# Optimization experiments

Hardware: AMD Instinct MI355X
Metric: run time of the kernel (lower is better)

Reference implementation:

```python
import jax, jax.numpy as jnp
import numpy as np

NEG_INF = -1e30


def setup_inputs() -> dict:
    key = jax.random.key(0)
    ks = jax.random.split(key, 7)
    B, D, LC, LQ = 32, 128, 2048, 256
    C = jax.random.normal(ks[0], (B, D, LC), dtype=jnp.float32)
    Q = jax.random.normal(ks[1], (B, D, LQ), dtype=jnp.float32)
    Cmask = jax.random.randint(ks[2], (B, LC), 0, 2, dtype=jnp.int32)
    Qmask = jax.random.randint(ks[3], (B, LQ), 0, 2, dtype=jnp.int32)
    w4C = jax.random.normal(ks[4], (D, 1), dtype=jnp.float32) * (6.0 / (D + 1)) ** 0.5
    w4Q = jax.random.normal(ks[5], (D, 1), dtype=jnp.float32) * (6.0 / (D + 1)) ** 0.5
    w4mlu = jax.random.normal(ks[6], (1, 1, D), dtype=jnp.float32) * (6.0 / (D + 1)) ** 0.5
    bias = jnp.zeros((1,), dtype=jnp.float32)
    return {"C": C, "Q": Q, "Cmask": Cmask, "Qmask": Qmask,
            "w4C": w4C, "w4Q": w4Q, "w4mlu": w4mlu, "bias": bias}


def reference(C, Q, Cmask, Qmask, w4C, w4Q, w4mlu, bias):
    # C: [B, D, Lc], Q: [B, D, Lq] -> transpose to token-major
    Ct = jnp.swapaxes(C, 1, 2)  # [B, Lc, D]
    Qt = jnp.swapaxes(Q, 1, 2)  # [B, Lq, D]
    # trilinear similarity S[b,i,j] = w4C.Ct[b,i] + w4Q.Qt[b,j] + (Ct[b,i]*w4mlu).Qt[b,j] + bias
    sub0 = Ct @ w4C                                   # [B, Lc, 1]
    sub1 = jnp.swapaxes(Qt @ w4Q, 1, 2)               # [B, 1, Lq]
    sub2 = jnp.einsum('bcd,bqd->bcq', Ct * w4mlu, Qt)  # [B, Lc, Lq]
    S = sub0 + sub1 + sub2 + bias                     # [B, Lc, Lq]
    Qm = Qmask.astype(jnp.float32)[:, None, :]        # [B, 1, Lq]
    Cm = Cmask.astype(jnp.float32)[:, :, None]        # [B, Lc, 1]
    S1 = jax.nn.softmax(S + NEG_INF * (1.0 - Qm), axis=2)  # row softmax over Lq
    S2 = jax.nn.softmax(S + NEG_INF * (1.0 - Cm), axis=1)  # col softmax over Lc
    A = S1 @ Qt                                       # [B, Lc, D]
    Bt = jnp.einsum('bcq,bkq->bck', S1, S2) @ Ct      # (S1 @ S2^T) @ C -> [B, Lc, D]
    out = jnp.concatenate([Ct, A, Ct * A, Ct * Bt], axis=2)  # [B, Lc, 4D]
    return jnp.swapaxes(out, 1, 2)  # [B, 4D, Lc]
```

## Files before the change

kernel.cpp:

```cpp
#include <hip/hip_runtime.h>
#include <cstdint>


#define NB 32
#define ND 128
#define NLC 2048
#define NLQ 256
#define FNEG (-1.0e30f)
#define ESHIFT 20.0f

typedef __attribute__((ext_vector_type(8))) short bf16x8;
typedef __attribute__((ext_vector_type(4))) float f32x4;
#define MFMA16(a, b, c) __builtin_amdgcn_mfma_f32_16x16x32_bf16(a, b, c, 0, 0, 0)

__device__ __forceinline__ short f2bf(float x) {
  union { float f; unsigned u; } v; v.f = x;
  unsigned r = (v.u + 0x7FFFu + ((v.u >> 16) & 1u)) >> 16;
  return (short)r;
}
__device__ __forceinline__ float bf2f(short x) {
  union { unsigned u; float f; } v; v.u = ((unsigned)(unsigned short)x) << 16;
  return v.f;
}

__global__ __launch_bounds__(256) void k_tr(const float* __restrict__ C,
                                            const float* __restrict__ Q,
                                            const float* __restrict__ w4C,
                                            const float* __restrict__ w4Q,
                                            const float* __restrict__ w4mlu,
                                            short* __restrict__ Cfr,
                                            short* __restrict__ Cafr,
                                            short* __restrict__ Qfr,
                                            short* __restrict__ Qbf,
                                            float* __restrict__ cqp,
                                            float* __restrict__ qqp,
                                            const int* __restrict__ Qmask,
                                            short* __restrict__ mskE) {
  __shared__ float T[32][66];
  const int b = blockIdx.z, d0 = blockIdx.y * 32;
  const int t = threadIdx.x;
  const bool isC = blockIdx.x < 32;
  const int i0 = (isC ? blockIdx.x : (blockIdx.x - 32)) * 64;
  const int L = isC ? NLC : NLQ;
  const float* in = isC ? C : Q;
#pragma unroll
  for (int rr = 0; rr < 2; ++rr) {
    int idx = t + rr * 256;
    int dd = idx >> 4, c4 = idx & 15;
    const float* src = in + ((size_t)b * ND + d0 + dd) * L + i0 + c4 * 4;
    float4 v = *(const float4*)src;
    T[dd][c4 * 4 + 0] = v.x;
    T[dd][c4 * 4 + 1] = v.y;
    T[dd][c4 * 4 + 2] = v.z;
    T[dd][c4 * 4 + 3] = v.w;
    if (!isC) {
      short4 o;
      o.x = f2bf(v.x); o.y = f2bf(v.y); o.z = f2bf(v.z); o.w = f2bf(v.w);
      *(short4*)(Qbf + ((size_t)b * ND + d0 + dd) * L + i0 + c4 * 4) = o;
    }
  }
  __syncthreads();
  if (t < 64) {
    const float* wd_ = isC ? w4C : w4Q;
    float s = 0.f;
#pragma unroll
    for (int dd = 0; dd < 32; ++dd) s = fmaf(T[dd][t], wd_[d0 + dd], s);
    (isC ? cqp : qqp)[((size_t)blockIdx.y * NB + b) * L + i0 + t] = s;
  }
  if (!isC && blockIdx.y == 0 && t < 64) {
    const int j = i0 + t;
    mskE[(size_t)b * NLQ + j] = Qmask[b * NLQ + j] ? (short)0xFFFF : (short)0;
  }
  if (isC) {
    const int dt_loc = t & 1, ic_loc = (t >> 1) & 1, lane = t >> 2;
    const int dd = dt_loc * 16 + (lane & 15);
    const int ibase = ic_loc * 32 + ((lane >> 4) & 3) * 8;
    bf16x8 pk;
#pragma unroll
    for (int k = 0; k < 8; ++k) pk[k] = f2bf(T[dd][ibase + k]);
    const size_t dtile = (size_t)((d0 >> 4) + dt_loc);
    const size_t ichunk = (size_t)((i0 >> 5) + ic_loc);
    *(bf16x8*)(Cafr + (((size_t)b * 8 + dtile) * (size_t)(NLC >> 5) + ichunk) * 512 +
               (size_t)lane * 8) = pk;
  }
  const int i = t >> 2, seg = t & 3;
  bf16x8 pack;
#pragma unroll
  for (int k = 0; k < 8; ++k) {
    int d = seg * 8 + k;
    float x = T[d][i];
    if (!isC) x *= w4mlu[d0 + d];
    pack[k] = f2bf(x);
  }
  {
    const size_t tile = (size_t)((i0 + i) >> 4);
    const int lane = seg * 16 + ((i0 + i) & 15);
    *(bf16x8*)((isC ? Cfr : Qfr) + ((size_t)b * (L >> 4) + tile) * 2048 +
               (size_t)(d0 >> 5) * 512 + (size_t)lane * 8) = pack;
  }
}

__global__ __launch_bounds__(1024) void k_MT(const short* __restrict__ Cfr,
                                             const short* __restrict__ Qfr,
                                             const short* __restrict__ Cafr,
                                             const int* __restrict__ Cmask,
                                             const float* __restrict__ cqp,
                                             const float* __restrict__ qqp,
                                             const float* __restrict__ bias,
                                             short* __restrict__ MTbf,
                                             short* __restrict__ E) {
  __shared__ short PTs[32 * 136];
  __shared__ float cspart[16][32];
  __shared__ float bc[32];
  __shared__ float mtred[8][2][64][4];
  const int flat = blockIdx.x;
  const int swz = (flat & 7) * 32 + (flat >> 3);
  const int b = swz >> 3, qt = (swz & 7) * 32;
  const int tid = threadIdx.x;
  const int w = tid >> 6, l = tid & 63, lm = l & 15, lk = l >> 4;
  const int qsub = w & 1, ioct = w >> 1;
  const int wd = w & 7, wh = w >> 3;
  const float bv = bias[0];

  bf16x8 aq[4];
  {
    const short* Qf = Qfr + ((size_t)b * 16 + (qt >> 4) + qsub) * 2048 + (size_t)l * 8;
#pragma unroll
    for (int kk = 0; kk < 4; ++kk) aq[kk] = *(const bf16x8*)(Qf + kk * 512);
  }
  float qqv[4];
#pragma unroll
  for (int r = 0; r < 4; ++r) {
    const size_t j = (size_t)b * NLQ + qt + qsub * 16 + lk * 4 + r;
    qqv[r] = qqp[j] + qqp[(size_t)NB * NLQ + j] + qqp[2 * (size_t)NB * NLQ + j] +
             qqp[3 * (size_t)NB * NLQ + j] + bv;
  }

  const int elane = (qsub * 2 + (lk >> 1)) * 16 + lm;
  short* Eb = E + (size_t)b * 128 * 4096 + (size_t)(qt >> 5) * 512 +
              (size_t)elane * 8 + (lk & 1) * 4;

  float csacc[4] = {0.f, 0.f, 0.f, 0.f};
  f32x4 accMT[2] = {{0.f, 0.f, 0.f, 0.f}, {0.f, 0.f, 0.f, 0.f}};
  for (int i0 = 0; i0 < NLC; i0 += 128) {
    {
      const int iCol = i0 + ioct * 16 + lm;
      const short* Cf = Cfr + ((size_t)b * 128 + (i0 >> 4) + ioct) * 2048 + (size_t)l * 8;
      f32x4 c = {0.f, 0.f, 0.f, 0.f};
#pragma unroll
      for (int kk = 0; kk < 4; ++kk)
        c = MFMA16(aq[kk], *(const bf16x8*)(Cf + kk * 512), c);
      const size_t ci = (size_t)b * NLC + iCol;
      const float cqb = cqp[ci] + cqp[(size_t)NB * NLC + ci] +
                        cqp[2 * (size_t)NB * NLC + ci] + cqp[3 * (size_t)NB * NLC + ci];
      const int cm = Cmask[b * NLC + iCol];
      short ev[4];
#pragma unroll
      for (int r = 0; r < 4; ++r) {
        float s = c[r] + cqb + qqv[r];
        float pu = __expf(s - ESHIFT);
        float pm = cm ? pu : 0.f;
        csacc[r] += pm;
        PTs[(qsub * 16 + lk * 4 + r) * 136 + ioct * 16 + lm] = f2bf(pm);
        ev[r] = f2bf(pu);
      }
      *(short4*)(Eb + (size_t)((i0 >> 4) + ioct) * 4096) = *(short4*)ev;
    }
    __syncthreads();
    const short* Arow = Cafr + (((size_t)b * 8 + wd) * 64 + (i0 >> 5)) * 512 + (size_t)l * 8;
#pragma unroll
    for (int ks2 = 0; ks2 < 2; ++ks2) {
      const int ks = wh * 2 + ks2;
      bf16x8 a = *(const bf16x8*)(Arow + ks * 512);
#pragma unroll
      for (int qs = 0; qs < 2; ++qs) {
        bf16x8 bb = *(const bf16x8*)&PTs[(qs * 16 + lm) * 136 + ks * 32 + lk * 8];
        accMT[qs] = MFMA16(a, bb, accMT[qs]);
      }
    }
    __syncthreads();
  }
  if (wh == 1) {
#pragma unroll
    for (int qs = 0; qs < 2; ++qs)
#pragma unroll
      for (int r = 0; r < 4; ++r) mtred[wd][qs][l][r] = accMT[qs][r];
  }
#pragma unroll
  for (int off = 1; off < 16; off <<= 1)
#pragma unroll
    for (int r = 0; r < 4; ++r) csacc[r] += __shfl_xor(csacc[r], off, 64);
  if (lm == 0) {
#pragma unroll
    for (int r = 0; r < 4; ++r) cspart[w][qsub * 16 + lk * 4 + r] = csacc[r];
  }
  __syncthreads();
  if (tid < 32) {
    const int base = (tid >> 4) & 1;
    float s = 0.f;
#pragma unroll
    for (int k2 = 0; k2 < 8; ++k2) s += cspart[k2 * 2 + base][tid];
    bc[tid] = 1.0f / s;
  }
  __syncthreads();
  if (wh == 0) {
#pragma unroll
    for (int qs = 0; qs < 2; ++qs) {
#pragma unroll
      for (int r = 0; r < 4; ++r) accMT[qs][r] += mtred[wd][qs][l][r];
      const float inv = bc[qs * 16 + lm];
#pragma unroll
      for (int r = 0; r < 4; ++r)
        MTbf[((size_t)b * ND + wd * 16 + lk * 4 + r) * NLQ + qt + qs * 16 + lm] =
            f2bf(accMT[qs][r] * inv);
    }
  }
}

__global__ __launch_bounds__(256) void k_PAB(const short* __restrict__ Cafr,
                                             const short* __restrict__ E,
                                             const short* __restrict__ mskE,
                                             const short* __restrict__ Qbf,
                                             const short* __restrict__ MTbf,
                                             float* __restrict__ out) {
  __shared__ __align__(16) char Bst[32768];
  const int flat = blockIdx.x;
  const int swz = (flat & 7) * 128 + (flat >> 3);
  const int b = swz >> 5, it = (swz & 31) * 64;
  const int tid = threadIdx.x;
  const int wi = tid >> 6, l = tid & 63, lm = l & 15, lk = l >> 4;

  bf16x8 afr[8];
  {
    const short* Ef = E + ((size_t)b * 128 + (it >> 4) + wi) * 4096 + (size_t)l * 8;
    const short* mb = mskE + (size_t)b * NLQ + lk * 8;
#pragma unroll
    for (int kk = 0; kk < 8; ++kk) {
      bf16x8 a = *(const bf16x8*)(Ef + kk * 512);
      bf16x8 m = *(const bf16x8*)(mb + kk * 32);
      afr[kk] = a & m;
    }
  }
  float rsum = 0.f;
#pragma unroll
  for (int kk = 0; kk < 8; ++kk)
#pragma unroll
    for (int e = 0; e < 8; ++e) rsum += bf2f(afr[kk][e]);
  rsum += __shfl_xor(rsum, 16, 64);
  rsum += __shfl_xor(rsum, 32, 64);
  float invr[4];
#pragma unroll
  for (int r = 0; r < 4; ++r)
    invr[r] = 1.0f / __shfl(rsum, (l & 48) + lk * 4 + r, 64);

  const short* Qp = Qbf + (size_t)b * ND * NLQ;
  const short* Mp = MTbf + (size_t)b * ND * NLQ;
  float* ob = out + (size_t)b * 4 * ND * NLC;
  const int iB = it + wi * 16 + lk * 4;
  const size_t cbase = ((size_t)b * 8 * 64 + (size_t)(iB >> 5)) * 512 +
                       (size_t)(((iB >> 3) & 3) * 16 + lm) * 8 + (size_t)(iB & 7);

  const int srow = tid >> 4, scol = tid & 15;
  const int wsw0 = (((scol * 2) ^ (srow & 7)) << 4);
  const int wsw1 = (((scol * 2 + 1) ^ (srow & 7)) << 4);
  const short* qsrc = Qp + (size_t)srow * NLQ + scol * 16;
  const short* msrc = Mp + (size_t)srow * NLQ + scol * 16;
  bf16x8 sq0, sq1, sm0, sm1;

#define LOADN(n0) { \
    const short* q_ = qsrc + (size_t)(n0) * 16 * NLQ; \
    const short* m_ = msrc + (size_t)(n0) * 16 * NLQ; \
    sq0 = *(const bf16x8*)q_;  sq1 = *(const bf16x8*)(q_ + 8); \
    sm0 = *(const bf16x8*)m_;  sm1 = *(const bf16x8*)(m_ + 8); }
#define WRITEN(buf) { \
    char* base_ = Bst + (buf) * 16384 + srow * 512; \
    *(bf16x8*)(base_ + wsw0) = sq0; *(bf16x8*)(base_ + wsw1) = sq1; \
    *(bf16x8*)(base_ + 8192 + wsw0) = sm0; *(bf16x8*)(base_ + 8192 + wsw1) = sm1; }

  LOADN(0); WRITEN(0);
  __syncthreads();
#pragma unroll
  for (int n0 = 0; n0 < 8; ++n0) {
    if (n0 < 7) LOADN(n0 + 1);
    const int d = n0 * 16 + lm;
    short4 cts = *(const short4*)&Cafr[cbase + (size_t)n0 * 64 * 512];
    const char* bq = Bst + (n0 & 1) * 16384 + lm * 512;
    f32x4 cA = {0.f, 0.f, 0.f, 0.f};
    f32x4 cB = {0.f, 0.f, 0.f, 0.f};
#pragma unroll
    for (int kk = 0; kk < 8; ++kk) {
      const int so = (((kk * 4 + lk) ^ (lm & 7)) << 4);
      cA = MFMA16(afr[kk], *(const bf16x8*)(bq + so), cA);
      cB = MFMA16(afr[kk], *(const bf16x8*)(bq + 8192 + so), cB);
    }
    if (n0 < 7) {
      WRITEN((n0 + 1) & 1);
      __syncthreads();
    }
    float4 ct;
    ct.x = bf2f(cts.x); ct.y = bf2f(cts.y); ct.z = bf2f(cts.z); ct.w = bf2f(cts.w);
    float4 av, ca, cb;
    av.x = cA[0] * invr[0]; av.y = cA[1] * invr[1];
    av.z = cA[2] * invr[2]; av.w = cA[3] * invr[3];
    ca.x = ct.x * av.x; ca.y = ct.y * av.y; ca.z = ct.z * av.z; ca.w = ct.w * av.w;
    cb.x = ct.x * cB[0] * invr[0]; cb.y = ct.y * cB[1] * invr[1];
    cb.z = ct.z * cB[2] * invr[2]; cb.w = ct.w * cB[3] * invr[3];
    float* o0 = ob + (size_t)d * NLC + iB;
    *(float4*)o0 = ct;
    *(float4*)(o0 + (size_t)128 * NLC) = av;
    *(float4*)(o0 + (size_t)256 * NLC) = ca;
    *(float4*)(o0 + (size_t)384 * NLC) = cb;
  }
#undef LOADN
#undef WRITEN
}

extern "C" void kernel_launch(void* const* d_in, const int* in_sizes, int n_in,
                              void* d_out, int out_size, void* d_ws, size_t ws_size,
                              hipStream_t stream) {
  const float* C = (const float*)d_in[0];
  const float* Q = (const float*)d_in[1];
  const int* Cmask = (const int*)d_in[2];
  const int* Qmask = (const int*)d_in[3];
  const float* w4C = (const float*)d_in[4];
  const float* w4Q = (const float*)d_in[5];
  const float* w4mlu = (const float*)d_in[6];
  const float* bias = (const float*)d_in[7];
  float* out = (float*)d_out;

  short* Cfr = (short*)d_ws;
  short* Cafr = Cfr + (size_t)NB * NLC * ND;
  short* Qfr = Cafr + (size_t)NB * NLC * ND;
  short* Qbf = Qfr + (size_t)NB * NLQ * ND;
  short* MTbf = Qbf + (size_t)NB * NLQ * ND;
  short* E = MTbf + (size_t)NB * ND * NLQ;
  short* mskE = E + (size_t)NB * NLC * NLQ;
  float* cqp = (float*)(mskE + (size_t)NB * NLQ);
  float* qqp = cqp + 4 * (size_t)NB * NLC;
  size_t need = (size_t)(qqp + 4 * NB * NLQ - (float*)d_ws) * sizeof(float);
  if (ws_size < need) return;

  k_tr<<<dim3(36, 4, NB), 256, 0, stream>>>(C, Q, w4C, w4Q, w4mlu, Cfr, Cafr, Qfr, Qbf,
                                            cqp, qqp, Qmask, mskE);
  k_MT<<<256, 1024, 0, stream>>>(Cfr, Qfr, Cafr, Cmask, cqp, qqp, bias, MTbf, E);
  k_PAB<<<1024, 256, 0, stream>>>(Cafr, E, mskE, Qbf, MTbf, out);
}
```

Baseline: 82.77 us.

## Double-buffer k_MT smem, prefetch fragments, and emit C passthrough from transpose kernel

Double-buffers the probability tile in shared memory so the per-iteration trailing barrier can be removed. It also prefetches the next C fragments and the Ca operands into registers before the barrier. The first output slice (the C passthrough) is now written directly in fp32 by the transpose kernel rather than by the final kernel, which is also more exact than the old bf16 round trip. The final kernel hoists its Ca loads ahead of the loop. The trade-off is more shared memory and registers, and extra write traffic moved into k_tr.

```diff
diff --git a/kernel.cpp b/kernel.cpp
--- a/kernel.cpp
+++ b/kernel.cpp
@@ -35,7 +35,8 @@
                                             float* __restrict__ cqp,
                                             float* __restrict__ qqp,
                                             const int* __restrict__ Qmask,
-                                            short* __restrict__ mskE) {
+                                            short* __restrict__ mskE,
+                                            float* __restrict__ out) {
   __shared__ float T[32][66];
   const int b = blockIdx.z, d0 = blockIdx.y * 32;
   const int t = threadIdx.x;
@@ -57,6 +58,8 @@
       short4 o;
       o.x = f2bf(v.x); o.y = f2bf(v.y); o.z = f2bf(v.z); o.w = f2bf(v.w);
       *(short4*)(Qbf + ((size_t)b * ND + d0 + dd) * L + i0 + c4 * 4) = o;
+    } else {
+      *(float4*)(out + ((size_t)b * 4 * ND + d0 + dd) * NLC + i0 + c4 * 4) = v;
     }
   }
   __syncthreads();
@@ -109,7 +112,7 @@
                                              const float* __restrict__ bias,
                                              short* __restrict__ MTbf,
                                              short* __restrict__ E) {
-  __shared__ short PTs[32 * 136];
+  __shared__ short PTs[2][32 * 136];
   __shared__ float cspart[16][32];
   __shared__ float bc[32];
   __shared__ float mtred[8][2][64][4];
@@ -140,16 +143,23 @@
   short* Eb = E + (size_t)b * 128 * 4096 + (size_t)(qt >> 5) * 512 +
               (size_t)elane * 8 + (lk & 1) * 4;
 
+  bf16x8 cf[4];
+  {
+    const short* Cf0 = Cfr + ((size_t)b * 128 + ioct) * 2048 + (size_t)l * 8;
+#pragma unroll
+    for (int kk = 0; kk < 4; ++kk) cf[kk] = *(const bf16x8*)(Cf0 + kk * 512);
+  }
+
   float csacc[4] = {0.f, 0.f, 0.f, 0.f};
   f32x4 accMT[2] = {{0.f, 0.f, 0.f, 0.f}, {0.f, 0.f, 0.f, 0.f}};
-  for (int i0 = 0; i0 < NLC; i0 += 128) {
+  for (int i0 = 0, it = 0; i0 < NLC; i0 += 128, ++it) {
+    const int p = it & 1;
+    short* PT = PTs[p];
     {
       const int iCol = i0 + ioct * 16 + lm;
-      const short* Cf = Cfr + ((size_t)b * 128 + (i0 >> 4) + ioct) * 2048 + (size_t)l * 8;
       f32x4 c = {0.f, 0.f, 0.f, 0.f};
 #pragma unroll
-      for (int kk = 0; kk < 4; ++kk)
-        c = MFMA16(aq[kk], *(const bf16x8*)(Cf + kk * 512), c);
+      for (int kk = 0; kk < 4; ++kk) c = MFMA16(aq[kk], cf[kk], c);
       const size_t ci = (size_t)b * NLC + iCol;
       const float cqb = cqp[ci] + cqp[(size_t)NB * NLC + ci] +
                         cqp[2 * (size_t)NB * NLC + ci] + cqp[3 * (size_t)NB * NLC + ci];
@@ -161,25 +171,35 @@
         float pu = __expf(s - ESHIFT);
         float pm = cm ? pu : 0.f;
         csacc[r] += pm;
-        PTs[(qsub * 16 + lk * 4 + r) * 136 + ioct * 16 + lm] = f2bf(pm);
+        PT[(qsub * 16 + lk * 4 + r) * 136 + ioct * 16 + lm] = f2bf(pm);
         ev[r] = f2bf(pu);
       }
       *(short4*)(Eb + (size_t)((i0 >> 4) + ioct) * 4096) = *(short4*)ev;
     }
+    bf16x8 a4[2];
+    {
+      const short* Arow = Cafr + (((size_t)b * 8 + wd) * 64 + (i0 >> 5)) * 512 +
+                          (size_t)(wh * 2) * 512 + (size_t)l * 8;
+      a4[0] = *(const bf16x8*)Arow;
+      a4[1] = *(const bf16x8*)(Arow + 512);
+    }
+    if (i0 + 128 < NLC) {
+      const short* Cfn = Cfr + ((size_t)b * 128 + (i0 >> 4) + 8 + ioct) * 2048 + (size_t)l * 8;
+#pragma unroll
+      for (int kk = 0; kk < 4; ++kk) cf[kk] = *(const bf16x8*)(Cfn + kk * 512);
+    }
     __syncthreads();
-    const short* Arow = Cafr + (((size_t)b * 8 + wd) * 64 + (i0 >> 5)) * 512 + (size_t)l * 8;
 #pragma unroll
     for (int ks2 = 0; ks2 < 2; ++ks2) {
       const int ks = wh * 2 + ks2;
-      bf16x8 a = *(const bf16x8*)(Arow + ks * 512);
 #pragma unroll
       for (int qs = 0; qs < 2; ++qs) {
-        bf16x8 bb = *(const bf16x8*)&PTs[(qs * 16 + lm) * 136 + ks * 32 + lk * 8];
-        accMT[qs] = MFMA16(a, bb, accMT[qs]);
+        bf16x8 bb = *(const bf16x8*)&PT[(qs * 16 + lm) * 136 + ks * 32 + lk * 8];
+        accMT[qs] = MFMA16(a4[ks2], bb, accMT[qs]);
       }
     }
-    __syncthreads();
-  }
+  }
+  __syncthreads();
   if (wh == 1) {
 #pragma unroll
     for (int qs = 0; qs < 2; ++qs)
@@ -253,12 +273,17 @@
   for (int r = 0; r < 4; ++r)
     invr[r] = 1.0f / __shfl(rsum, (l & 48) + lk * 4 + r, 64);
 
+  const int iB = it + wi * 16 + lk * 4;
+  const size_t cbase = ((size_t)b * 8 * 64 + (size_t)(iB >> 5)) * 512 +
+                       (size_t)(((iB >> 3) & 3) * 16 + lm) * 8 + (size_t)(iB & 7);
+  short4 cts[8];
+#pragma unroll
+  for (int n0 = 0; n0 < 8; ++n0)
+    cts[n0] = *(const short4*)&Cafr[cbase + (size_t)n0 * 64 * 512];
+
   const short* Qp = Qbf + (size_t)b * ND * NLQ;
   const short* Mp = MTbf + (size_t)b * ND * NLQ;
   float* ob = out + (size_t)b * 4 * ND * NLC;
-  const int iB = it + wi * 16 + lk * 4;
-  const size_t cbase = ((size_t)b * 8 * 64 + (size_t)(iB >> 5)) * 512 +
-                       (size_t)(((iB >> 3) & 3) * 16 + lm) * 8 + (size_t)(iB & 7);
 
   const int srow = tid >> 4, scol = tid & 15;
   const int wsw0 = (((scol * 2) ^ (srow & 7)) << 4);
@@ -283,7 +308,6 @@
   for (int n0 = 0; n0 < 8; ++n0) {
     if (n0 < 7) LOADN(n0 + 1);
     const int d = n0 * 16 + lm;
-    short4 cts = *(const short4*)&Cafr[cbase + (size_t)n0 * 64 * 512];
     const char* bq = Bst + (n0 & 1) * 16384 + lm * 512;
     f32x4 cA = {0.f, 0.f, 0.f, 0.f};
     f32x4 cB = {0.f, 0.f, 0.f, 0.f};
@@ -298,7 +322,8 @@
       __syncthreads();
     }
     float4 ct;
-    ct.x = bf2f(cts.x); ct.y = bf2f(cts.y); ct.z = bf2f(cts.z); ct.w = bf2f(cts.w);
+    ct.x = bf2f(cts[n0].x); ct.y = bf2f(cts[n0].y);
+    ct.z = bf2f(cts[n0].z); ct.w = bf2f(cts[n0].w);
     float4 av, ca, cb;
     av.x = cA[0] * invr[0]; av.y = cA[1] * invr[1];
     av.z = cA[2] * invr[2]; av.w = cA[3] * invr[3];
@@ -306,7 +331,6 @@
     cb.x = ct.x * cB[0] * invr[0]; cb.y = ct.y * cB[1] * invr[1];
     cb.z = ct.z * cB[2] * invr[2]; cb.w = ct.w * cB[3] * invr[3];
     float* o0 = ob + (size_t)d * NLC + iB;
-    *(float4*)o0 = ct;
     *(float4*)(o0 + (size_t)128 * NLC) = av;
     *(float4*)(o0 + (size_t)256 * NLC) = ca;
     *(float4*)(o0 + (size_t)384 * NLC) = cb;
@@ -341,7 +365,7 @@
   if (ws_size < need) return;
 
   k_tr<<<dim3(36, 4, NB), 256, 0, stream>>>(C, Q, w4C, w4Q, w4mlu, Cfr, Cafr, Qfr, Qbf,
-                                            cqp, qqp, Qmask, mskE);
+                                            cqp, qqp, Qmask, mskE, out);
   k_MT<<<256, 1024, 0, stream>>>(Cfr, Qfr, Cafr, Cmask, cqp, qqp, bias, MTbf, E);
   k_PAB<<<1024, 256, 0, stream>>>(Cafr, E, mskE, Qbf, MTbf, out);
 }
```

Measured after the change: 75.06 us. -9.3%, faster.
